# Performance work log

Measured on AMD Instinct MI355X. Metric: run time of the kernel, lower is better.

Reference implementation:

```python
import jax, jax.numpy as jnp
import numpy as np

B, S, D, H = 2, 2048, 1024, 16
DK = D // H

def setup_inputs() -> dict:
    key = jax.random.key(0)
    ks = jax.random.split(key, 9)
    def lin(k, fan_in):
        bound = 1.0 / np.sqrt(fan_in)
        kw, kb = jax.random.split(k)
        w = jax.random.uniform(kw, (D, D), jnp.float32, -bound, bound)
        b = jax.random.uniform(kb, (D,), jnp.float32, -bound, bound)
        return w, b
    Wq_w, Wq_b = lin(ks[0], D)
    Wk_w, Wk_b = lin(ks[1], D)
    Wv_w, Wv_b = lin(ks[2], D)
    Wo_w, Wo_b = lin(ks[3], D)
    x = jax.random.normal(ks[4], (B, S, D), jnp.float32)
    mask = jnp.ones((B, 1, 1, S), jnp.int32)
    return {"x": x, "mask": mask,
            "Wq_w": Wq_w, "Wq_b": Wq_b, "Wk_w": Wk_w, "Wk_b": Wk_b,
            "Wv_w": Wv_w, "Wv_b": Wv_b, "Wo_w": Wo_w, "Wo_b": Wo_b}

def reference(x, mask, Wq_w, Wq_b, Wk_w, Wk_b, Wv_w, Wv_b, Wo_w, Wo_b):
    b, s, d = x.shape
    def split_heads(t):  # [B,S,D] -> [B,H,S,DK]
        return t.reshape(b, s, H, DK).transpose(0, 2, 1, 3)
    Q = split_heads(x @ Wq_w.T + Wq_b)
    K = split_heads(x @ Wk_w.T + Wk_b)
    V = split_heads(x @ Wv_w.T + Wv_b)
    scale = 1.0 / jnp.sqrt(jnp.float32(DK))
    scores = jnp.einsum('bhqd,bhkd->bhqk', Q, K) * scale  # [B,H,S,S]
    scores = jnp.where(mask == 0, jnp.float32(-1e9), scores)
    attn = jax.nn.softmax(scores, axis=-1)
    context = jnp.einsum('bhqk,bhkd->bhqd', attn, V)  # [B,H,S,DK]
    context = context.transpose(0, 2, 1, 3).reshape(b, s, d)
    return context @ Wo_w.T + Wo_b
```

## Files before the change

### kernel.cpp

```cpp
#include <hip/hip_runtime.h>
#include <hip/hip_bf16.h>


#define DEV __device__ __forceinline__

typedef __bf16 bf16_t;
typedef __bf16 bf16x8 __attribute__((ext_vector_type(8)));
typedef float f32x4 __attribute__((ext_vector_type(4)));

constexpr int Ss = 2048, Dd = 1024, Hh = 16, DKk = 64;

DEV void gload_lds16(const void* g, void* l) {
  __builtin_amdgcn_global_load_lds(
      (__attribute__((address_space(1))) void*)(g),
      (__attribute__((address_space(3))) void*)(l), 16, 0, 0);
}

DEV bf16_t f2b(float v) { return (bf16_t)v; }

DEV void cvt16_core(const float* src, bf16_t* dst) {
  const float4* s4 = (const float4*)src;
  float4 a = s4[0], b = s4[1], c = s4[2], d = s4[3];
  bf16x8 lo = {f2b(a.x), f2b(a.y), f2b(a.z), f2b(a.w), f2b(b.x), f2b(b.y), f2b(b.z), f2b(b.w)};
  bf16x8 hi = {f2b(c.x), f2b(c.y), f2b(c.z), f2b(c.w), f2b(d.x), f2b(d.y), f2b(d.z), f2b(d.w)};
  *(bf16x8*)dst = lo;
  *(bf16x8*)(dst + 8) = hi;
}

__global__ __launch_bounds__(256) void cvt16(const float* __restrict__ x,
                                             bf16_t* __restrict__ xb) {
  size_t i = ((size_t)blockIdx.x * 256 + threadIdx.x) * 16;
  cvt16_core(x + i, xb + i);
}

__global__ __launch_bounds__(256) void cvt_all(
    const float* __restrict__ x,
    const float* __restrict__ wq, const float* __restrict__ wk,
    const float* __restrict__ wv, const float* __restrict__ wo,
    bf16_t* __restrict__ xb, bf16_t* __restrict__ Wb) {
  size_t i = ((size_t)blockIdx.x * 256 + threadIdx.x) * 16;
  const size_t XN = (size_t)4 << 20;
  if (i < XN) {
    cvt16_core(x + i, xb + i);
  } else {
    size_t j = i - XN;
    int z = (int)(j >> 20);
    size_t o = j & (((size_t)1 << 20) - 1);
    const float* s = (z == 0) ? wq : ((z == 1) ? wk : ((z == 2) ? wv : wo));
    cvt16_core(s + o, Wb + j);
  }
}

template <bool WB16>
__global__ __launch_bounds__(256) void gemm_qkv(
    const bf16_t* __restrict__ A,
    const float* __restrict__ W0, const float* __restrict__ W1, const float* __restrict__ W2,
    const bf16_t* __restrict__ Wb,
    const float* __restrict__ b0, const float* __restrict__ b1, const float* __restrict__ b2,
    bf16_t* __restrict__ o0, bf16_t* __restrict__ o1, bf16_t* __restrict__ o2) {
  const int z = blockIdx.z;
  const float* Wf = (z == 0) ? W0 : ((z == 1) ? W1 : W2);
  const bf16_t* Wbf = Wb + (size_t)z * (1u << 20);
  const float* bias = (z == 0) ? b0 : ((z == 1) ? b1 : b2);
  bf16_t* out = (z == 0) ? o0 : ((z == 1) ? o1 : o2);

  __shared__ __align__(16) bf16_t As[128 * 32];
  __shared__ __align__(16) bf16_t Ws[128 * 32];

  const int tid = threadIdx.x;
  const int lane = tid & 63, w = tid >> 6;
  const int quad = lane >> 4, c = lane & 15;
  const int wm = w >> 1, wn = w & 1;
  const int m0 = blockIdx.y * 128, n0 = blockIdx.x * 128;
  const int trow = tid >> 1, tcol = (tid & 1) * 16;
  const int srow = lane >> 2, scol = (lane & 3) * 8;

  const f32x4 vzero = {0.f, 0.f, 0.f, 0.f};
  f32x4 acc[4][4];
  for (int i = 0; i < 4; i++)
    for (int j = 0; j < 4; j++) acc[i][j] = vzero;

  for (int k0 = 0; k0 < 1024; k0 += 32) {
    for (int r = 0; r < 2; r++) {
      int row = r * 64 + w * 16;
      gload_lds16(&A[(size_t)(m0 + row + srow) * 1024 + k0 + scol], &As[row * 32]);
      if (WB16)
        gload_lds16(&Wbf[(size_t)(n0 + row + srow) * 1024 + k0 + scol], &Ws[row * 32]);
    }
    if (!WB16)
      cvt16_core(&Wf[(size_t)(n0 + trow) * 1024 + k0 + tcol], &Ws[trow * 32 + tcol]);
    __syncthreads();

    bf16x8 af[4], bfr[4];
    for (int i = 0; i < 4; i++)
      af[i] = *(const bf16x8*)&As[(wm * 64 + i * 16 + c) * 32 + quad * 8];
    for (int j = 0; j < 4; j++)
      bfr[j] = *(const bf16x8*)&Ws[(wn * 64 + j * 16 + c) * 32 + quad * 8];
    for (int i = 0; i < 4; i++)
      for (int j = 0; j < 4; j++)
        acc[i][j] = __builtin_amdgcn_mfma_f32_16x16x32_bf16(af[i], bfr[j], acc[i][j], 0, 0, 0);
    __syncthreads();
  }

  for (int j = 0; j < 4; j++) {
    int n = n0 + wn * 64 + j * 16 + c;
    float bv = bias[n];
    for (int i = 0; i < 4; i++) {
      int mbase = m0 + wm * 64 + i * 16 + quad * 4;
      for (int r = 0; r < 4; r++) {
        int m = mbase + r;
        float v = acc[i][j][r] + bv;
        int b_ = m >> 11, s_ = m & 2047, h_ = n >> 6, dk_ = n & 63;
        if (z < 2)
          out[((size_t)(b_ * Hh + h_) * Ss + s_) * DKk + dk_] = f2b(v);
        else
          out[((size_t)(b_ * Hh + h_) * DKk + dk_) * Ss + s_] = f2b(v);
      }
    }
  }
}

__global__ __launch_bounds__(256) void attn_fwd(
    const bf16_t* __restrict__ Q, const bf16_t* __restrict__ K,
    const bf16_t* __restrict__ Vt, const int* __restrict__ mask,
    bf16_t* __restrict__ ctx) {
  __shared__ __align__(16) bf16_t Ks[64 * 64];
  __shared__ __align__(16) bf16_t Vts[64 * 64];
  __shared__ __align__(16) bf16_t Ps[4][32 * 64];

  const int tid = threadIdx.x, lane = tid & 63, w = tid >> 6;
  const int quad = lane >> 4, c = lane & 15;
  const int c7 = c & 7;
  const int bh = blockIdx.y, b_ = bh >> 4, h_ = bh & 15;
  const int q0 = blockIdx.x * 128 + w * 32;
  const size_t head = (size_t)bh * Ss * DKk;

  bf16x8 qf[2][2];
  for (int mi = 0; mi < 2; mi++)
    for (int ks = 0; ks < 2; ks++)
      qf[mi][ks] = *(const bf16x8*)&Q[head + (size_t)(q0 + mi * 16 + c) * DKk + ks * 32 + quad * 8];

  const bf16_t oneb = f2b(1.0f);
  const bf16x8 ones = {oneb, oneb, oneb, oneb, oneb, oneb, oneb, oneb};

  const f32x4 vzero = {0.f, 0.f, 0.f, 0.f};
  f32x4 o[2][4];
  for (int mi = 0; mi < 2; mi++)
    for (int j = 0; j < 4; j++) o[mi][j] = vzero;
  f32x4 ol[2] = {vzero, vzero};

  const int sr = lane >> 3;
  const int gc = (lane & 7) ^ sr;

  for (int kt = 0; kt < Ss / 64; kt++) {
    __syncthreads();
    for (int r = 0; r < 2; r++) {
      int row = r * 32 + w * 8;
      gload_lds16(&K[head + (size_t)(kt * 64 + row + sr) * 64 + gc * 8], &Ks[row * 64]);
      gload_lds16(&Vt[head + (size_t)(row + sr) * Ss + kt * 64 + gc * 8], &Vts[row * 64]);
    }
    __syncthreads();

    f32x4 sc[2][4];
    for (int mi = 0; mi < 2; mi++)
      for (int ni = 0; ni < 4; ni++) sc[mi][ni] = vzero;
    for (int ks = 0; ks < 2; ks++) {
      int pc = ((ks * 4 + quad) ^ c7) * 8;
      for (int ni = 0; ni < 4; ni++) {
        bf16x8 kf = *(const bf16x8*)&Ks[(ni * 16 + c) * 64 + pc];
        sc[0][ni] = __builtin_amdgcn_mfma_f32_16x16x32_bf16(qf[0][ks], kf, sc[0][ni], 0, 0, 0);
        sc[1][ni] = __builtin_amdgcn_mfma_f32_16x16x32_bf16(qf[1][ks], kf, sc[1][ni], 0, 0, 0);
      }
    }

    for (int ni = 0; ni < 4; ni++) {
      int mk = mask[b_ * Ss + kt * 64 + ni * 16 + c];
      for (int mi = 0; mi < 2; mi++)
        for (int r = 0; r < 4; r++) {
          float p = __expf(sc[mi][ni][r] * 0.125f);
          sc[mi][ni][r] = mk ? p : 0.f;
        }
    }

    for (int mi = 0; mi < 2; mi++)
      for (int ni = 0; ni < 4; ni++)
        for (int r = 0; r < 4; r++) {
          int ql = mi * 16 + quad * 4 + r;
          int chunk = (ni * 2 + (c >> 3)) ^ (ql & 7);
          Ps[w][ql * 64 + chunk * 8 + c7] = f2b(sc[mi][ni][r]);
        }

    for (int ks = 0; ks < 2; ks++) {
      int pc = ((ks * 4 + quad) ^ c7) * 8;
      bf16x8 pf0 = *(const bf16x8*)&Ps[w][(c)*64 + pc];
      bf16x8 pf1 = *(const bf16x8*)&Ps[w][(16 + c) * 64 + pc];
      for (int j = 0; j < 4; j++) {
        bf16x8 vf = *(const bf16x8*)&Vts[(j * 16 + c) * 64 + pc];
        o[0][j] = __builtin_amdgcn_mfma_f32_16x16x32_bf16(pf0, vf, o[0][j], 0, 0, 0);
        o[1][j] = __builtin_amdgcn_mfma_f32_16x16x32_bf16(pf1, vf, o[1][j], 0, 0, 0);
      }
      ol[0] = __builtin_amdgcn_mfma_f32_16x16x32_bf16(pf0, ones, ol[0], 0, 0, 0);
      ol[1] = __builtin_amdgcn_mfma_f32_16x16x32_bf16(pf1, ones, ol[1], 0, 0, 0);
    }
  }

  for (int mi = 0; mi < 2; mi++) {
    float inv[4];
    for (int r = 0; r < 4; r++) inv[r] = 1.0f / ol[mi][r];
    for (int j = 0; j < 4; j++)
      for (int r = 0; r < 4; r++) {
        int s_ = q0 + mi * 16 + quad * 4 + r;
        ctx[((size_t)(b_ * Ss + s_)) * Dd + h_ * 64 + j * 16 + c] =
            f2b(o[mi][j][r] * inv[r]);
      }
  }
}

template <bool WB16>
__global__ __launch_bounds__(256) void gemm_out(
    const bf16_t* __restrict__ A, const float* __restrict__ Wf,
    const bf16_t* __restrict__ Wb, const float* __restrict__ bias,
    float* __restrict__ out) {
  __shared__ __align__(16) bf16_t As[64 * 32];
  __shared__ __align__(16) bf16_t Ws[128 * 32];

  const int tid = threadIdx.x;
  const int lane = tid & 63, w = tid >> 6;
  const int quad = lane >> 4, c = lane & 15;
  const int wm = w >> 1, wn = w & 1;
  const int m0 = blockIdx.y * 64, n0 = blockIdx.x * 128;
  const int trow = tid >> 1, tcol = (tid & 1) * 16;
  const int srow = lane >> 2, scol = (lane & 3) * 8;

  const f32x4 vzero = {0.f, 0.f, 0.f, 0.f};
  f32x4 acc[2][4];
  for (int i = 0; i < 2; i++)
    for (int j = 0; j < 4; j++) acc[i][j] = vzero;

  for (int k0 = 0; k0 < 1024; k0 += 32) {
    gload_lds16(&A[(size_t)(m0 + w * 16 + srow) * 1024 + k0 + scol], &As[(w * 16) * 32]);
    if (WB16) {
      for (int r = 0; r < 2; r++) {
        int row = r * 64 + w * 16;
        gload_lds16(&Wb[(size_t)(n0 + row + srow) * 1024 + k0 + scol], &Ws[row * 32]);
      }
    } else {
      cvt16_core(&Wf[(size_t)(n0 + trow) * 1024 + k0 + tcol], &Ws[trow * 32 + tcol]);
    }
    __syncthreads();

    bf16x8 af[2], bfr[4];
    for (int i = 0; i < 2; i++)
      af[i] = *(const bf16x8*)&As[(wm * 32 + i * 16 + c) * 32 + quad * 8];
    for (int j = 0; j < 4; j++)
      bfr[j] = *(const bf16x8*)&Ws[(wn * 64 + j * 16 + c) * 32 + quad * 8];
    for (int i = 0; i < 2; i++)
      for (int j = 0; j < 4; j++)
        acc[i][j] = __builtin_amdgcn_mfma_f32_16x16x32_bf16(af[i], bfr[j], acc[i][j], 0, 0, 0);
    __syncthreads();
  }

  for (int j = 0; j < 4; j++) {
    int n = n0 + wn * 64 + j * 16 + c;
    float bv = bias[n];
    for (int i = 0; i < 2; i++) {
      int mbase = m0 + wm * 32 + i * 16 + quad * 4;
      for (int r = 0; r < 4; r++)
        out[(size_t)(mbase + r) * 1024 + n] = acc[i][j][r] + bv;
    }
  }
}

extern "C" void kernel_launch(void* const* d_in, const int* in_sizes, int n_in,
                              void* d_out, int out_size, void* d_ws, size_t ws_size,
                              hipStream_t stream) {
  const float* x  = (const float*)d_in[0];
  const int* mask = (const int*)d_in[1];
  const float* Wq = (const float*)d_in[2];
  const float* bq = (const float*)d_in[3];
  const float* Wk = (const float*)d_in[4];
  const float* bk = (const float*)d_in[5];
  const float* Wv = (const float*)d_in[6];
  const float* bv = (const float*)d_in[7];
  const float* Wo = (const float*)d_in[8];
  const float* bo = (const float*)d_in[9];
  float* out = (float*)d_out;

  bf16_t* ws = (bf16_t*)d_ws;
  const size_t QKV_ELEMS = (size_t)2 * Hh * Ss * DKk;
  bf16_t* xb  = ws;
  bf16_t* Qb  = ws + QKV_ELEMS;
  bf16_t* Kb  = ws + 2 * QKV_ELEMS;
  bf16_t* Vt  = ws + 3 * QKV_ELEMS;
  bf16_t* Wb  = ws + 4 * QKV_ELEMS;
  bf16_t* ctx = xb;

  const bool wb16 = ws_size >= (size_t)40 * 1024 * 1024;

  if (wb16) {
    cvt_all<<<dim3(2048), 256, 0, stream>>>(x, Wq, Wk, Wv, Wo, xb, Wb);
    gemm_qkv<true><<<dim3(8, 32, 3), 256, 0, stream>>>(
        xb, Wq, Wk, Wv, Wb, bq, bk, bv, Qb, Kb, Vt);
  } else {
    cvt16<<<dim3(1024), 256, 0, stream>>>(x, xb);
    gemm_qkv<false><<<dim3(8, 32, 3), 256, 0, stream>>>(
        xb, Wq, Wk, Wv, ws , bq, bk, bv, Qb, Kb, Vt);
  }
  attn_fwd<<<dim3(Ss / 128, 2 * Hh), 256, 0, stream>>>(Qb, Kb, Vt, mask, ctx);
  if (wb16)
    gemm_out<true><<<dim3(8, 64), 256, 0, stream>>>(ctx, Wo, Wb + 3 * (1u << 20), bo, out);
  else
    gemm_out<false><<<dim3(8, 64), 256, 0, stream>>>(ctx, Wo, ws , bo, out);
}
```

Measured before the change: 220.4 us.

## Double-buffer K/V tiles in attention and vectorize transposed V stores

The attention kernel now keeps two LDS buffers for K and V^T. It prefetches the next tile with global_load_lds while computing on the current one, which also cuts the loop to a single barrier per iteration. Mask values are prefetched one tile ahead into registers. The projection epilogue writes transposed V as packed 4-element bf16 stores instead of scalar stores. The cost is doubled K/V LDS use, which may reduce occupancy.

```diff
diff --git a/kernel.cpp b/kernel.cpp
--- a/kernel.cpp
+++ b/kernel.cpp
@@ -5,6 +5,7 @@
 #define DEV __device__ __forceinline__
 
 typedef __bf16 bf16_t;
+typedef __bf16 bf16x4 __attribute__((ext_vector_type(4)));
 typedef __bf16 bf16x8 __attribute__((ext_vector_type(8)));
 typedef float f32x4 __attribute__((ext_vector_type(4)));
 
@@ -107,14 +108,16 @@
     float bv = bias[n];
     for (int i = 0; i < 4; i++) {
       int mbase = m0 + wm * 64 + i * 16 + quad * 4;
-      for (int r = 0; r < 4; r++) {
-        int m = mbase + r;
-        float v = acc[i][j][r] + bv;
-        int b_ = m >> 11, s_ = m & 2047, h_ = n >> 6, dk_ = n & 63;
-        if (z < 2)
-          out[((size_t)(b_ * Hh + h_) * Ss + s_) * DKk + dk_] = f2b(v);
-        else
-          out[((size_t)(b_ * Hh + h_) * DKk + dk_) * Ss + s_] = f2b(v);
+      int b_ = mbase >> 11, s_ = mbase & 2047;
+      int h_ = n >> 6, dk_ = n & 63;
+      if (z < 2) {
+        for (int r = 0; r < 4; r++)
+          out[((size_t)(b_ * Hh + h_) * Ss + (s_ + r)) * DKk + dk_] =
+              f2b(acc[i][j][r] + bv);
+      } else {
+        bf16x4 pk;
+        for (int r = 0; r < 4; r++) pk[r] = f2b(acc[i][j][r] + bv);
+        *(bf16x4*)&out[((size_t)(b_ * Hh + h_) * DKk + dk_) * Ss + s_] = pk;
       }
     }
   }
@@ -124,8 +127,8 @@
     const bf16_t* __restrict__ Q, const bf16_t* __restrict__ K,
     const bf16_t* __restrict__ Vt, const int* __restrict__ mask,
     bf16_t* __restrict__ ctx) {
-  __shared__ __align__(16) bf16_t Ks[64 * 64];
-  __shared__ __align__(16) bf16_t Vts[64 * 64];
+  __shared__ __align__(16) bf16_t Ks[2][64 * 64];
+  __shared__ __align__(16) bf16_t Vts[2][64 * 64];
   __shared__ __align__(16) bf16_t Ps[4][32 * 64];
 
   const int tid = threadIdx.x, lane = tid & 63, w = tid >> 6;
@@ -134,11 +137,26 @@
   const int bh = blockIdx.y, b_ = bh >> 4, h_ = bh & 15;
   const int q0 = blockIdx.x * 128 + w * 32;
   const size_t head = (size_t)bh * Ss * DKk;
+  const int* maskb = mask + b_ * Ss;
+
+  const int sr = lane >> 3;
+  const int gc = (lane & 7) ^ sr;
+
+  {
+    for (int r = 0; r < 2; r++) {
+      int row = r * 32 + w * 8;
+      gload_lds16(&K[head + (size_t)(row + sr) * 64 + gc * 8], &Ks[0][row * 64]);
+      gload_lds16(&Vt[head + (size_t)(row + sr) * Ss + gc * 8], &Vts[0][row * 64]);
+    }
+  }
 
   bf16x8 qf[2][2];
   for (int mi = 0; mi < 2; mi++)
     for (int ks = 0; ks < 2; ks++)
       qf[mi][ks] = *(const bf16x8*)&Q[head + (size_t)(q0 + mi * 16 + c) * DKk + ks * 32 + quad * 8];
+
+  int mk[4];
+  for (int ni = 0; ni < 4; ni++) mk[ni] = maskb[ni * 16 + c];
 
   const bf16_t oneb = f2b(1.0f);
   const bf16x8 ones = {oneb, oneb, oneb, oneb, oneb, oneb, oneb, oneb};
@@ -149,17 +167,24 @@
     for (int j = 0; j < 4; j++) o[mi][j] = vzero;
   f32x4 ol[2] = {vzero, vzero};
 
-  const int sr = lane >> 3;
-  const int gc = (lane & 7) ^ sr;
-
-  for (int kt = 0; kt < Ss / 64; kt++) {
-    __syncthreads();
-    for (int r = 0; r < 2; r++) {
-      int row = r * 32 + w * 8;
-      gload_lds16(&K[head + (size_t)(kt * 64 + row + sr) * 64 + gc * 8], &Ks[row * 64]);
-      gload_lds16(&Vt[head + (size_t)(row + sr) * Ss + kt * 64 + gc * 8], &Vts[row * 64]);
-    }
-    __syncthreads();
+  constexpr int NT = Ss / 64;
+  for (int kt = 0; kt < NT; kt++) {
+    const int cur = kt & 1;
+    __syncthreads();
+
+    if (kt + 1 < NT) {
+      int nxt = cur ^ 1;
+      for (int r = 0; r < 2; r++) {
+        int row = r * 32 + w * 8;
+        gload_lds16(&K[head + (size_t)((kt + 1) * 64 + row + sr) * 64 + gc * 8],
+                    &Ks[nxt][row * 64]);
+        gload_lds16(&Vt[head + (size_t)(row + sr) * Ss + (kt + 1) * 64 + gc * 8],
+                    &Vts[nxt][row * 64]);
+      }
+    }
+    int mkn[4];
+    if (kt + 1 < NT)
+      for (int ni = 0; ni < 4; ni++) mkn[ni] = maskb[(kt + 1) * 64 + ni * 16 + c];
 
     f32x4 sc[2][4];
     for (int mi = 0; mi < 2; mi++)
@@ -167,18 +192,17 @@
     for (int ks = 0; ks < 2; ks++) {
       int pc = ((ks * 4 + quad) ^ c7) * 8;
       for (int ni = 0; ni < 4; ni++) {
-        bf16x8 kf = *(const bf16x8*)&Ks[(ni * 16 + c) * 64 + pc];
+        bf16x8 kf = *(const bf16x8*)&Ks[cur][(ni * 16 + c) * 64 + pc];
         sc[0][ni] = __builtin_amdgcn_mfma_f32_16x16x32_bf16(qf[0][ks], kf, sc[0][ni], 0, 0, 0);
         sc[1][ni] = __builtin_amdgcn_mfma_f32_16x16x32_bf16(qf[1][ks], kf, sc[1][ni], 0, 0, 0);
       }
     }
 
     for (int ni = 0; ni < 4; ni++) {
-      int mk = mask[b_ * Ss + kt * 64 + ni * 16 + c];
       for (int mi = 0; mi < 2; mi++)
         for (int r = 0; r < 4; r++) {
           float p = __expf(sc[mi][ni][r] * 0.125f);
-          sc[mi][ni][r] = mk ? p : 0.f;
+          sc[mi][ni][r] = mk[ni] ? p : 0.f;
         }
     }
 
@@ -195,13 +219,15 @@
       bf16x8 pf0 = *(const bf16x8*)&Ps[w][(c)*64 + pc];
       bf16x8 pf1 = *(const bf16x8*)&Ps[w][(16 + c) * 64 + pc];
       for (int j = 0; j < 4; j++) {
-        bf16x8 vf = *(const bf16x8*)&Vts[(j * 16 + c) * 64 + pc];
+        bf16x8 vf = *(const bf16x8*)&Vts[cur][(j * 16 + c) * 64 + pc];
         o[0][j] = __builtin_amdgcn_mfma_f32_16x16x32_bf16(pf0, vf, o[0][j], 0, 0, 0);
         o[1][j] = __builtin_amdgcn_mfma_f32_16x16x32_bf16(pf1, vf, o[1][j], 0, 0, 0);
       }
       ol[0] = __builtin_amdgcn_mfma_f32_16x16x32_bf16(pf0, ones, ol[0], 0, 0, 0);
       ol[1] = __builtin_amdgcn_mfma_f32_16x16x32_bf16(pf1, ones, ol[1], 0, 0, 0);
     }
+
+    for (int ni = 0; ni < 4; ni++) mk[ni] = mkn[ni];
   }
 
   for (int mi = 0; mi < 2; mi++) {
```

After: 220.1 us. Within noise of the previous version (-0.1%).
